# Optimization experiments

Measured on AMD Instinct MI355X. Metric: run time of the kernel, lower is better.

The kernel has to match this reference:

```python
import jax, jax.numpy as jnp
import numpy as np

D_MODEL = 1024
NUM_HEADS = 16
D_K = D_MODEL // NUM_HEADS
WINDOW = 256


def setup_inputs() -> dict:
    key = jax.random.key(0)
    ks = jax.random.split(key, 11)
    B, S, D = 2, 2048, D_MODEL
    scale = 1.0 / np.sqrt(D)
    inp = {
        "q": jax.random.normal(ks[0], (B, S, D), jnp.float32),
        "k": jax.random.normal(ks[1], (B, S, D), jnp.float32),
        "v": jax.random.normal(ks[2], (B, S, D), jnp.float32),
        "Wq": jax.random.normal(ks[3], (D, D), jnp.float32) * scale,
        "bq": jnp.zeros((D,), jnp.float32),
        "Wk": jax.random.normal(ks[4], (D, D), jnp.float32) * scale,
        "bk": jnp.zeros((D,), jnp.float32),
        "Wv": jax.random.normal(ks[5], (D, D), jnp.float32) * scale,
        "bv": jnp.zeros((D,), jnp.float32),
        "Wo": jax.random.normal(ks[6], (D, D), jnp.float32) * scale,
        "bo": jnp.zeros((D,), jnp.float32),
    }
    return inp


def _split_heads(x):
    B, S, _ = x.shape
    return x.reshape(B, S, NUM_HEADS, D_K).transpose(0, 2, 1, 3)  # [B,H,S,d_k]


def reference(q, k, v, Wq, bq, Wk, bk, Wv, bv, Wo, bo):
    B, S, D = q.shape
    qh = _split_heads(q @ Wq + bq)
    kh = _split_heads(k @ Wk + bk)
    vh = _split_heads(v @ Wv + bv)

    # dense scores then sliding-window band mask (|i-j| <= WINDOW), as in SparseAttention
    scores = jnp.einsum("bhqd,bhkd->bhqk", qh, kh) / jnp.sqrt(jnp.float32(D_K))
    idx = jnp.arange(S)
    band = jnp.abs(idx[:, None] - idx[None, :]) <= WINDOW  # [S,S]
    scores = jnp.where(band[None, None], scores, -jnp.inf)
    attn = jax.nn.softmax(scores, axis=-1)

    out = jnp.einsum("bhqk,bhkd->bhqd", attn, vh)
    out = out.transpose(0, 2, 1, 3).reshape(B, S, D)  # combine heads
    out = out @ Wo + bo
    return out, attn
```

## Files before the change

### kernel.cpp

```cpp
#include <hip/hip_runtime.h>


constexpr int Bb = 2, Ss = 2048, Dd = 1024, Hh = 16, WINw = 256;
constexpr size_t XS_SLAB = (size_t)4096 * 2048;
constexpr size_t WT_SLAB = (size_t)1024 * 2048;
constexpr size_t QB_SLAB = (size_t)4096 * 1024;
constexpr size_t ATTN_BYTES = (size_t)Bb * Hh * Ss * Ss * 4;

typedef short s16x8 __attribute__((ext_vector_type(8)));
typedef float f32x4 __attribute__((ext_vector_type(4)));

typedef __attribute__((address_space(3))) unsigned int lds_uint;
typedef const __attribute__((address_space(1))) unsigned int gbl_uint;

__device__ __forceinline__ void gld_lds16(const void* g, void* l) {
  __builtin_amdgcn_global_load_lds((gbl_uint*)g, (lds_uint*)l, 16, 0, 0);
}

__device__ __forceinline__ void lgkm_barrier() {
  asm volatile("s_waitcnt lgkmcnt(0)" ::: "memory");
  __builtin_amdgcn_s_barrier();
}

__device__ inline unsigned short f2bf(float x) {
  unsigned u = __float_as_uint(x);
  u += 0x7fff + ((u >> 16) & 1);
  return (unsigned short)(u >> 16);
}
__device__ inline float bf2f(unsigned short h) {
  return __uint_as_float(((unsigned)h) << 16);
}

__global__ __launch_bounds__(256) void convert_xw(
    const float* __restrict__ x0, const float* __restrict__ x1,
    const float* __restrict__ x2, unsigned short* __restrict__ Xs,
    const float* __restrict__ w0, const float* __restrict__ w1,
    const float* __restrict__ w2, const float* __restrict__ w3,
    unsigned short* __restrict__ Wt) {
  __shared__ float T[64][65];
  const int id = blockIdx.x;
  const int t = threadIdx.x;
  if (id < 12288) {
    int z = id >> 12;
    int bx = id & 4095;
    const float* src = z == 0 ? x0 : (z == 1 ? x1 : x2);
    unsigned short* dst = Xs + (size_t)z * XS_SLAB;
    size_t idx = ((size_t)bx * 256 + t) * 4;
    int r = (int)(idx >> 10);
    int c = (int)(idx & 1023);
    f32x4 v = *(const f32x4*)&src[idx];
    unsigned short hi[4], lo[4];
#pragma unroll
    for (int i = 0; i < 4; ++i) {
      float vi = v[i];
      hi[i] = f2bf(vi);
      lo[i] = f2bf(vi - bf2f(hi[i]));
    }
    ushort4 h4 = {hi[0], hi[1], hi[2], hi[3]};
    ushort4 l4 = {lo[0], lo[1], lo[2], lo[3]};
    *(ushort4*)&dst[(size_t)r * 2048 + c] = h4;
    *(ushort4*)&dst[(size_t)r * 2048 + 1024 + c] = l4;
  } else {
    int wid = id - 12288;
    int z = wid >> 8;
    int by = (wid >> 4) & 15;
    int bx = wid & 15;
    const float* W = z == 0 ? w0 : (z == 1 ? w1 : (z == 2 ? w2 : w3));
    unsigned short* dst = Wt + (size_t)z * WT_SLAB;
    int k0 = by * 64, n0 = bx * 64;
#pragma unroll
    for (int i = 0; i < 4; ++i) {
      int row = (t >> 4) + i * 16;
      int c4 = (t & 15) * 4;
      f32x4 v = *(const f32x4*)&W[(size_t)(k0 + row) * 1024 + n0 + c4];
      T[row][c4 + 0] = v[0]; T[row][c4 + 1] = v[1];
      T[row][c4 + 2] = v[2]; T[row][c4 + 3] = v[3];
    }
    __syncthreads();
    int n = t >> 2;
    int kc = (t & 3) * 16;
    unsigned short hi[16], lo[16];
#pragma unroll
    for (int j = 0; j < 16; ++j) {
      float x = T[kc + j][n];
      hi[j] = f2bf(x);
      lo[j] = f2bf(x - bf2f(hi[j]));
    }
    size_t base = (size_t)(n0 + n) * 2048 + k0 + kc;
#pragma unroll
    for (int j4 = 0; j4 < 4; ++j4) {
      ushort4 h4 = {hi[j4 * 4], hi[j4 * 4 + 1], hi[j4 * 4 + 2], hi[j4 * 4 + 3]};
      ushort4 l4 = {lo[j4 * 4], lo[j4 * 4 + 1], lo[j4 * 4 + 2], lo[j4 * 4 + 3]};
      *(ushort4*)&dst[base + j4 * 4] = h4;
      *(ushort4*)&dst[base + 1024 + j4 * 4] = l4;
    }
  }
}

__global__ __launch_bounds__(256, 3) void gemm_qkv(
    const unsigned short* __restrict__ Abase,
    const unsigned short* __restrict__ Wtbase,
    unsigned short* __restrict__ Cbase, const float* __restrict__ bb0,
    const float* __restrict__ bb1, const float* __restrict__ bb2,
    float* __restrict__ attnz) {
  __shared__ s16x8 As[2][512];
  __shared__ s16x8 Bs[2][512];
  int z = blockIdx.z;
  const unsigned short* A = Abase + (size_t)z * XS_SLAB;
  const unsigned short* Wt = Wtbase + (size_t)z * WT_SLAB;
  const float* bias = z == 0 ? bb0 : (z == 1 ? bb1 : bb2);
  const float scl = (z == 0) ? 0.125f : 1.0f;

  const int t = threadIdx.x;
  const int lane = t & 63, wave = t >> 6;
  const int wm = wave & 1, wn = wave >> 1;

  const int flat = blockIdx.x + (blockIdx.y << 3);
  const int swz = (flat & 7) * 32 + (flat >> 3);
  const int bm = (swz >> 3) * 128, bn = (swz & 7) * 128;

  const int flat3 = flat + (z << 8);
  const size_t zbase = (size_t)(flat3 * 4 + wave) * 196608;
  char* const az = (char*)attnz;
  const f32x4 zv = {0.f, 0.f, 0.f, 0.f};

  f32x4 acc[4][4] = {};

  const int s0 = t, s1 = t + 256;
  const int r0 = s0 >> 2, c0 = (s0 & 3) ^ ((r0 >> 1) & 3);
  const int r1 = s1 >> 2, c1 = (s1 & 3) ^ ((r1 >> 1) & 3);
  const unsigned short* A0 = A + (size_t)(bm + r0) * 2048 + c0 * 8;
  const unsigned short* A1 = A + (size_t)(bm + r1) * 2048 + c1 * 8;
  const unsigned short* B0 = Wt + (size_t)(bn + r0) * 2048 + c0 * 8;
  const unsigned short* B1 = Wt + (size_t)(bn + r1) * 2048 + c1 * 8;

  const int m15 = lane & 15, q = lane >> 4;

  gld_lds16(A0, &As[0][wave * 64]);
  gld_lds16(A1, &As[0][256 + wave * 64]);
  gld_lds16(B0, &Bs[0][wave * 64]);
  gld_lds16(B1, &Bs[0][256 + wave * 64]);
  __syncthreads();

  int cur = 0;
  for (int kb = 0; kb < 3072; kb += 32) {
    const int kn = kb + 32;
    if (kn < 3072) {
      int asrc = kn < 1024 ? kn : kn - 1024;
      int wsrc = kn < 2048 ? kn : kn - 2048;
      gld_lds16(A0 + asrc, &As[cur ^ 1][wave * 64]);
      gld_lds16(A1 + asrc, &As[cur ^ 1][256 + wave * 64]);
      gld_lds16(B0 + wsrc, &Bs[cur ^ 1][wave * 64]);
      gld_lds16(B1 + wsrc, &Bs[cur ^ 1][256 + wave * 64]);
    }

    {
      size_t off = zbase + (size_t)(kb >> 5) * 2048 + (size_t)(lane << 4);
      if (off < ATTN_BYTES) __builtin_nontemporal_store(zv, (f32x4*)(az + off));
      off += 1024;
      if (off < ATTN_BYTES) __builtin_nontemporal_store(zv, (f32x4*)(az + off));
    }

    s16x8 af[4], bf[4];
#pragma unroll
    for (int mt = 0; mt < 4; ++mt) {
      int r = wm * 64 + mt * 16 + m15;
      af[mt] = As[cur][r * 4 + (q ^ ((r >> 1) & 3))];
    }
#pragma unroll
    for (int nt = 0; nt < 4; ++nt) {
      int r = wn * 64 + nt * 16 + m15;
      bf[nt] = Bs[cur][r * 4 + (q ^ ((r >> 1) & 3))];
    }
#pragma unroll
    for (int mt = 0; mt < 4; ++mt)
#pragma unroll
      for (int nt = 0; nt < 4; ++nt)
        acc[mt][nt] = __builtin_amdgcn_mfma_f32_16x16x32_bf16(
            af[mt], bf[nt], acc[mt][nt], 0, 0, 0);

    if (kn < 3072) {
      __syncthreads();
      cur ^= 1;
    }
  }

#pragma unroll
  for (int nt = 0; nt < 4; ++nt) {
    int col = bn + wn * 64 + nt * 16 + m15;
    float bv = bias[col];
#pragma unroll
    for (int mt = 0; mt < 4; ++mt) {
      int rowb = bm + wm * 64 + mt * 16 + q * 4;
#pragma unroll
      for (int i = 0; i < 4; ++i) {
        float val = (acc[mt][nt][i] + bv) * scl;
        (Cbase + (size_t)z * QB_SLAB)[(size_t)(rowb + i) * 1024 + col] =
            f2bf(val);
      }
    }
  }
}

__global__ __launch_bounds__(256, 2) void gemm_out(
    const unsigned short* __restrict__ A,
    const unsigned short* __restrict__ Wt,
    float* __restrict__ C, const float* __restrict__ bias) {
  __shared__ s16x8 As[2][256];
  __shared__ s16x8 Bs[2][512];
  const int t = threadIdx.x;
  const int lane = t & 63, wave = t >> 6;
  const int wm = wave & 1, wn = wave >> 1;

  const int flat = blockIdx.x + (blockIdx.y << 3);
  const int swz = (flat & 7) * 64 + (flat >> 3);
  const int bm = (swz >> 3) * 64, bn = (swz & 7) * 128;

  f32x4 acc[2][4] = {};

  const int ra = t >> 2, ca = (t & 3) ^ ((ra >> 1) & 3);
  const int s0 = t, s1 = t + 256;
  const int r0 = s0 >> 2, c0 = (s0 & 3) ^ ((r0 >> 1) & 3);
  const int r1 = s1 >> 2, c1 = (s1 & 3) ^ ((r1 >> 1) & 3);
  const unsigned short* Ap = A + (size_t)(bm + ra) * 2048 + ca * 8;
  const unsigned short* B0 = Wt + (size_t)(bn + r0) * 2048 + c0 * 8;
  const unsigned short* B1 = Wt + (size_t)(bn + r1) * 2048 + c1 * 8;

  const int m15 = lane & 15, q = lane >> 4;

  gld_lds16(Ap, &As[0][wave * 64]);
  gld_lds16(B0, &Bs[0][wave * 64]);
  gld_lds16(B1, &Bs[0][256 + wave * 64]);
  __syncthreads();

  int cur = 0;
  for (int kb = 0; kb < 3072; kb += 32) {
    const int kn = kb + 32;
    if (kn < 3072) {
      int asrc = kn < 1024 ? kn : kn - 1024;
      int wsrc = kn < 2048 ? kn : kn - 2048;
      gld_lds16(Ap + asrc, &As[cur ^ 1][wave * 64]);
      gld_lds16(B0 + wsrc, &Bs[cur ^ 1][wave * 64]);
      gld_lds16(B1 + wsrc, &Bs[cur ^ 1][256 + wave * 64]);
    }

    s16x8 af[2], bf[4];
#pragma unroll
    for (int mt = 0; mt < 2; ++mt) {
      int r = wm * 32 + mt * 16 + m15;
      af[mt] = As[cur][r * 4 + (q ^ ((r >> 1) & 3))];
    }
#pragma unroll
    for (int nt = 0; nt < 4; ++nt) {
      int r = wn * 64 + nt * 16 + m15;
      bf[nt] = Bs[cur][r * 4 + (q ^ ((r >> 1) & 3))];
    }
#pragma unroll
    for (int mt = 0; mt < 2; ++mt)
#pragma unroll
      for (int nt = 0; nt < 4; ++nt)
        acc[mt][nt] = __builtin_amdgcn_mfma_f32_16x16x32_bf16(
            af[mt], bf[nt], acc[mt][nt], 0, 0, 0);

    if (kn < 3072) {
      __syncthreads();
      cur ^= 1;
    }
  }

#pragma unroll
  for (int nt = 0; nt < 4; ++nt) {
    int col = bn + wn * 64 + nt * 16 + m15;
    float bv = bias[col];
#pragma unroll
    for (int mt = 0; mt < 2; ++mt) {
      int rowb = bm + wm * 32 + mt * 16 + q * 4;
#pragma unroll
      for (int i = 0; i < 4; ++i) {
        __builtin_nontemporal_store(
            acc[mt][nt][i] + bv, &C[(size_t)(rowb + i) * 1024 + col]);
      }
    }
  }
}

__global__ __launch_bounds__(256) void transpose_v(
    const unsigned short* __restrict__ Vb, unsigned short* __restrict__ Vt) {
  __shared__ unsigned short T[64][88];
  const int b = blockIdx.z, h = blockIdx.y, s0 = blockIdx.x * 64;
  const int t = threadIdx.x;
  {
    int row = t >> 2, part = t & 3;
    const unsigned short* src =
        Vb + (size_t)(b * Ss + s0 + row) * 1024 + h * 64 + part * 16;
    s16x8 v0 = *(const s16x8*)src;
    s16x8 v1 = *(const s16x8*)(src + 8);
    *(s16x8*)&T[row][part * 16] = v0;
    *(s16x8*)&T[row][part * 16 + 8] = v1;
  }
  __syncthreads();
  {
    int d = t & 63, sw = t >> 6;
    unsigned short tmp[16];
#pragma unroll
    for (int i = 0; i < 16; ++i) tmp[i] = T[sw * 16 + i][d];
    unsigned short* dst =
        Vt + ((size_t)((b * Hh + h) * 64 + d)) * 2048 + s0 + sw * 16;
    *(s16x8*)dst = *(const s16x8*)&tmp[0];
    *(s16x8*)(dst + 8) = *(const s16x8*)&tmp[8];
  }
}

constexpr int SW3 = 556;
__global__ __launch_bounds__(256) void attn_v5(
    const unsigned short* __restrict__ Qb, const unsigned short* __restrict__ Kb,
    const unsigned short* __restrict__ Vt, float* __restrict__ attn,
    unsigned short* __restrict__ XsAO) {
  __shared__ float P[16 * SW3];
  const int t = threadIdx.x;
  const int lane = t & 63, wave = t >> 6;
  const int m15 = lane & 15, quad = lane >> 4;
  const int bid = blockIdx.x;
  const int qt = bid & 127, h = (bid >> 7) & 15, b = bid >> 11;
  const int q0 = qt * 16;
  int jlo = q0 - WINw; if (jlo < 0) jlo = 0;
  int jhi = q0 + 15 + WINw; if (jhi > Ss - 1) jhi = Ss - 1;
  const int ncols = jhi - jlo + 1;
  const int ntiles = ncols >> 4;

  {
    const unsigned short* qrow =
        Qb + (size_t)(b * Ss + q0 + m15) * 1024 + h * 64 + quad * 8;
    s16x8 aq0 = *(const s16x8*)qrow;
    s16x8 aq1 = *(const s16x8*)(qrow + 32);
    for (int nt = wave; nt < ntiles; nt += 4) {
      const unsigned short* krow =
          Kb + (size_t)(b * Ss + jlo + nt * 16 + m15) * 1024 + h * 64 + quad * 8;
      s16x8 b0 = *(const s16x8*)krow;
      s16x8 b1 = *(const s16x8*)(krow + 32);
      f32x4 c = {0.f, 0.f, 0.f, 0.f};
      __builtin_amdgcn_s_setprio(1);
      c = __builtin_amdgcn_mfma_f32_16x16x32_bf16(aq0, b0, c, 0, 0, 0);
      c = __builtin_amdgcn_mfma_f32_16x16x32_bf16(aq1, b1, c, 0, 0, 0);
      __builtin_amdgcn_s_setprio(0);
      float* pp = &P[(quad * 4) * SW3 + nt * 16 + m15];
#pragma unroll
      for (int i = 0; i < 4; ++i) pp[i * SW3] = c[i];
    }
  }
  lgkm_barrier();

  {
#pragma unroll
    for (int ri = 0; ri < 4; ++ri) {
      const int r = wave * 4 + ri;
      const int qq = q0 + r;
      int lo = qq - WINw; if (lo < 0) lo = 0;
      int hi = qq + WINw; if (hi > Ss - 1) hi = Ss - 1;
      const int clo = lo - jlo, chi = hi - jlo;
      float sv[9];
      bool ib[9];
      float m = -1e30f;
#pragma unroll
      for (int k2 = 0; k2 < 9; ++k2) {
        int c = k2 * 64 + lane;
        bool inb = (c >= clo) && (c <= chi);
        ib[k2] = inb;
        float vv = inb ? P[r * SW3 + c] : -1e30f;
        sv[k2] = vv;
        m = fmaxf(m, vv);
      }
#pragma unroll
      for (int off = 32; off; off >>= 1) m = fmaxf(m, __shfl_xor(m, off, 64));
      float e[9], l = 0.f;
#pragma unroll
      for (int k2 = 0; k2 < 9; ++k2) { e[k2] = __expf(sv[k2] - m); l += e[k2]; }
#pragma unroll
      for (int off = 32; off; off >>= 1) l += __shfl_xor(l, off, 64);
      const float inv = 1.f / l;
#pragma unroll
      for (int k2 = 0; k2 < 9; ++k2) {
        int c = k2 * 64 + lane;
        if (c < 544) P[r * SW3 + c] = ib[k2] ? e[k2] * inv : 0.f;
      }
      float* arow = attn + ((size_t)((b * Hh + h) * Ss + qq)) * Ss + jlo;
#pragma unroll
      for (int i = 0; i < 3; ++i) {
        int c = i * 256 + lane * 4;
        if (c < ncols) {
          f32x4 v = *(const f32x4*)&P[r * SW3 + c];
          __builtin_nontemporal_store(v, (f32x4*)&arow[c]);
        }
      }
    }
  }
  lgkm_barrier();

  {
    const int ntk = (ncols + 31) >> 5;
    const unsigned short* vtrow =
        Vt + ((size_t)((b * Hh + h) * 64 + wave * 16 + m15)) * 2048 + jlo +
        quad * 8;
    f32x4 o = {0.f, 0.f, 0.f, 0.f};
    for (int ks = 0; ks < ntk; ++ks) {
      const float* pa = &P[m15 * SW3 + ks * 32 + quad * 8];
      f32x4 p0 = *(const f32x4*)pa;
      f32x4 p1 = *(const f32x4*)(pa + 4);
      s16x8 af;
#pragma unroll
      for (int i = 0; i < 4; ++i) af[i] = (short)f2bf(p0[i]);
#pragma unroll
      for (int i = 0; i < 4; ++i) af[4 + i] = (short)f2bf(p1[i]);
      s16x8 bf = *(const s16x8*)(vtrow + ks * 32);
      __builtin_amdgcn_s_setprio(1);
      o = __builtin_amdgcn_mfma_f32_16x16x32_bf16(af, bf, o, 0, 0, 0);
      __builtin_amdgcn_s_setprio(0);
    }
    const int dcol = h * 64 + wave * 16 + m15;
#pragma unroll
    for (int i = 0; i < 4; ++i) {
      int row = q0 + quad * 4 + i;
      unsigned short hi = f2bf(o[i]);
      unsigned short lo = f2bf(o[i] - bf2f(hi));
      unsigned short* dst = XsAO + (size_t)(b * Ss + row) * 2048 + dcol;
      dst[0] = hi;
      dst[1024] = lo;
    }
  }
}

extern "C" void kernel_launch(void* const* d_in, const int* in_sizes, int n_in,
                              void* d_out, int out_size, void* d_ws,
                              size_t ws_size, hipStream_t stream) {
  const float* q  = (const float*)d_in[0];
  const float* k  = (const float*)d_in[1];
  const float* v  = (const float*)d_in[2];
  const float* Wq = (const float*)d_in[3];
  const float* bq = (const float*)d_in[4];
  const float* Wk = (const float*)d_in[5];
  const float* bk = (const float*)d_in[6];
  const float* Wv = (const float*)d_in[7];
  const float* bv = (const float*)d_in[8];
  const float* Wo = (const float*)d_in[9];
  const float* bo = (const float*)d_in[10];

  float* out = (float*)d_out;
  float* attn = out + (size_t)Bb * Ss * Dd;

  unsigned short* Xs   = (unsigned short*)d_ws;
  unsigned short* XsAO = Xs + 3 * XS_SLAB;
  unsigned short* Wt   = XsAO + XS_SLAB;
  unsigned short* Qb   = Wt + 4 * WT_SLAB;
  unsigned short* Kb   = Qb + QB_SLAB;
  unsigned short* Vb   = Kb + QB_SLAB;
  unsigned short* Vt   = Vb + QB_SLAB;

  hipLaunchKernelGGL(convert_xw, dim3(12288 + 1024), dim3(256), 0, stream,
                     q, k, v, Xs, Wq, Wk, Wv, Wo, Wt);
  hipLaunchKernelGGL(gemm_qkv, dim3(8, 32, 3), dim3(256), 0, stream,
                     Xs, Wt, Qb, bq, bk, bv, attn);
  hipLaunchKernelGGL(transpose_v, dim3(32, 16, 2), dim3(256), 0, stream,
                     Vb, Vt);
  hipLaunchKernelGGL(attn_v5, dim3(Bb * Hh * (Ss / 16)), dim3(256), 0, stream,
                     Qb, Kb, Vt, attn, XsAO);
  hipLaunchKernelGGL(gemm_out, dim3(8, 64, 1), dim3(256), 0, stream,
                     XsAO, Wt + 3 * WT_SLAB, out, bo);
}
```

Measured before the change: 779.3 us.

## Relax GEMM barrier waits, remap attention blocks, and store bf16 probabilities in LDS

In the QKV GEMM, the full __syncthreads is replaced by a partial vmcnt(2) wait so the two in-flight zero-fill stores of the attention matrix need not drain before each barrier. The zero stores become unconditional by clamping out-of-range offsets, and a sched barrier is added. In the attention kernel, block IDs are remapped so neighbouring blocks cover different batch/head slices. Softmax now writes bf16 probabilities to LDS and streams the fp32 values straight to global memory, which removes the LDS readback and the per-step conversion in the PV loop. The trade-offs are scalar global stores in place of 16-byte vector stores, plus redundant writes to the clamped last address.

```diff
diff --git a/kernel.cpp b/kernel.cpp
--- a/kernel.cpp
+++ b/kernel.cpp
@@ -145,7 +145,8 @@
   int cur = 0;
   for (int kb = 0; kb < 3072; kb += 32) {
     const int kn = kb + 32;
-    if (kn < 3072) {
+    const bool more = (kn < 3072);
+    if (more) {
       int asrc = kn < 1024 ? kn : kn - 1024;
       int wsrc = kn < 2048 ? kn : kn - 2048;
       gld_lds16(A0 + asrc, &As[cur ^ 1][wave * 64]);
@@ -153,12 +154,15 @@
       gld_lds16(B0 + wsrc, &Bs[cur ^ 1][wave * 64]);
       gld_lds16(B1 + wsrc, &Bs[cur ^ 1][256 + wave * 64]);
     }
+    __builtin_amdgcn_sched_barrier(0);
 
     {
-      size_t off = zbase + (size_t)(kb >> 5) * 2048 + (size_t)(lane << 4);
-      if (off < ATTN_BYTES) __builtin_nontemporal_store(zv, (f32x4*)(az + off));
-      off += 1024;
-      if (off < ATTN_BYTES) __builtin_nontemporal_store(zv, (f32x4*)(az + off));
+      size_t off0 = zbase + (size_t)(kb >> 5) * 2048 + (size_t)(lane << 4);
+      size_t off1 = off0 + 1024;
+      if (off0 >= ATTN_BYTES) off0 = ATTN_BYTES - 16;
+      if (off1 >= ATTN_BYTES) off1 = ATTN_BYTES - 16;
+      __builtin_nontemporal_store(zv, (f32x4*)(az + off0));
+      __builtin_nontemporal_store(zv, (f32x4*)(az + off1));
     }
 
     s16x8 af[4], bf[4];
@@ -179,8 +183,9 @@
         acc[mt][nt] = __builtin_amdgcn_mfma_f32_16x16x32_bf16(
             af[mt], bf[nt], acc[mt][nt], 0, 0, 0);
 
-    if (kn < 3072) {
-      __syncthreads();
+    if (more) {
+      asm volatile("s_waitcnt vmcnt(2) lgkmcnt(0)" ::: "memory");
+      __builtin_amdgcn_s_barrier();
       cur ^= 1;
     }
   }
@@ -312,7 +317,7 @@
 }
 
 constexpr int SW3 = 556;
-__global__ __launch_bounds__(256) void attn_v5(
+__global__ __launch_bounds__(256) void attn_v6(
     const unsigned short* __restrict__ Qb, const unsigned short* __restrict__ Kb,
     const unsigned short* __restrict__ Vt, float* __restrict__ attn,
     unsigned short* __restrict__ XsAO) {
@@ -320,7 +325,8 @@
   const int t = threadIdx.x;
   const int lane = t & 63, wave = t >> 6;
   const int m15 = lane & 15, quad = lane >> 4;
-  const int bid = blockIdx.x;
+  const int bid0 = blockIdx.x;
+  const int bid = (bid0 & 7) * 512 + (bid0 >> 3);
   const int qt = bid & 127, h = (bid >> 7) & 15, b = bid >> 11;
   const int q0 = qt * 16;
   int jlo = q0 - WINw; if (jlo < 0) jlo = 0;
@@ -378,19 +384,14 @@
 #pragma unroll
       for (int off = 32; off; off >>= 1) l += __shfl_xor(l, off, 64);
       const float inv = 1.f / l;
+      unsigned short* pb = (unsigned short*)&P[r * SW3];
+      float* arow = attn + ((size_t)((b * Hh + h) * Ss + qq)) * Ss + jlo;
 #pragma unroll
       for (int k2 = 0; k2 < 9; ++k2) {
         int c = k2 * 64 + lane;
-        if (c < 544) P[r * SW3 + c] = ib[k2] ? e[k2] * inv : 0.f;
-      }
-      float* arow = attn + ((size_t)((b * Hh + h) * Ss + qq)) * Ss + jlo;
-#pragma unroll
-      for (int i = 0; i < 3; ++i) {
-        int c = i * 256 + lane * 4;
-        if (c < ncols) {
-          f32x4 v = *(const f32x4*)&P[r * SW3 + c];
-          __builtin_nontemporal_store(v, (f32x4*)&arow[c]);
-        }
+        float w = ib[k2] ? e[k2] * inv : 0.f;
+        if (c < 544) pb[c] = f2bf(w);
+        if (c < ncols) __builtin_nontemporal_store(w, &arow[c]);
       }
     }
   }
@@ -402,15 +403,9 @@
         Vt + ((size_t)((b * Hh + h) * 64 + wave * 16 + m15)) * 2048 + jlo +
         quad * 8;
     f32x4 o = {0.f, 0.f, 0.f, 0.f};
+    const unsigned short* pbrow = (const unsigned short*)&P[m15 * SW3];
     for (int ks = 0; ks < ntk; ++ks) {
-      const float* pa = &P[m15 * SW3 + ks * 32 + quad * 8];
-      f32x4 p0 = *(const f32x4*)pa;
-      f32x4 p1 = *(const f32x4*)(pa + 4);
-      s16x8 af;
-#pragma unroll
-      for (int i = 0; i < 4; ++i) af[i] = (short)f2bf(p0[i]);
-#pragma unroll
-      for (int i = 0; i < 4; ++i) af[4 + i] = (short)f2bf(p1[i]);
+      s16x8 af = *(const s16x8*)&pbrow[ks * 32 + quad * 8];
       s16x8 bf = *(const s16x8*)(vtrow + ks * 32);
       __builtin_amdgcn_s_setprio(1);
       o = __builtin_amdgcn_mfma_f32_16x16x32_bf16(af, bf, o, 0, 0, 0);
@@ -461,7 +456,7 @@
                      Xs, Wt, Qb, bq, bk, bv, attn);
   hipLaunchKernelGGL(transpose_v, dim3(32, 16, 2), dim3(256), 0, stream,
                      Vb, Vt);
-  hipLaunchKernelGGL(attn_v5, dim3(Bb * Hh * (Ss / 16)), dim3(256), 0, stream,
+  hipLaunchKernelGGL(attn_v6, dim3(Bb * Hh * (Ss / 16)), dim3(256), 0, stream,
                      Qb, Kb, Vt, attn, XsAO);
   hipLaunchKernelGGL(gemm_out, dim3(8, 64, 1), dim3(256), 0, stream,
                      XsAO, Wt + 3 * WT_SLAB, out, bo);
```

Result: slower. 945.3 us (+21.3%).
